# Kernel optimization log

Measured on AMD Instinct MI355X. Metric: run time of the kernel, lower is better.

Reference implementation:

```python
import jax, jax.numpy as jnp
import numpy as np

N, E, D_IN, D_H, D_OUT = 50000, 800000, 128, 128, 40
EPS = 1e-5


def setup_inputs() -> dict:
    key = jax.random.key(0)
    ks = jax.random.split(key, 12)
    x = jax.random.normal(ks[0], (N, D_IN), dtype=jnp.float32)
    edge_index = jax.random.randint(ks[1], (2, E), 0, N, dtype=jnp.int32)
    s = 1.0 / np.sqrt(D_H)
    return {
        "x": x,
        "edge_index": edge_index,
        "W1": jax.random.normal(ks[2], (D_IN, D_H), jnp.float32) * s,
        "b1": jnp.zeros((D_H,), jnp.float32),
        "W2": jax.random.normal(ks[3], (D_H, D_H), jnp.float32) * s,
        "b2": jnp.zeros((D_H,), jnp.float32),
        "g1": jnp.ones((D_H,), jnp.float32),
        "be1": jnp.zeros((D_H,), jnp.float32),
        "g2": jnp.ones((D_H,), jnp.float32),
        "be2": jnp.zeros((D_H,), jnp.float32),
        "g3": jnp.ones((D_H,), jnp.float32),
        "be3": jnp.zeros((D_H,), jnp.float32),
        "Wm": jax.random.normal(ks[4], (D_H, D_OUT), jnp.float32) * s,
        "bm": jnp.zeros((D_OUT,), jnp.float32),
    }


def _gcn_conv(x, W, b, src, dst, dinv):
    # GCNConv: x' = D^{-1/2}(A+I)D^{-1/2} (x W) + b
    xw = x @ W                                   # [N, H]
    coef = dinv[src] * dinv[dst]                 # [E]
    agg = jax.ops.segment_sum(xw[src] * coef[:, None], dst, num_segments=x.shape[0])
    agg = agg + xw * (dinv * dinv)[:, None]      # self-loop term
    return agg + b


def _bn(x, g, b):
    # BatchNorm1d in training mode: biased batch statistics over nodes
    m = jnp.mean(x, axis=0)
    v = jnp.var(x, axis=0)
    return g * (x - m) * jax.lax.rsqrt(v + EPS) + b


def reference(x, edge_index, W1, b1, W2, b2, g1, be1, g2, be2, g3, be3, Wm, bm):
    src, dst = edge_index[0], edge_index[1]
    # degree with self-loops (GCN symmetric normalization, computed on dst/col)
    deg = 1.0 + jax.ops.segment_sum(jnp.ones((E,), jnp.float32), dst, num_segments=N)
    dinv = jax.lax.rsqrt(deg)
    h = _gcn_conv(x, W1, b1, src, dst, dinv)
    h = jax.nn.relu(_bn(h, g1, be1))            # dropout is identity in eval
    h = _gcn_conv(h, W2, b2, src, dst, dinv)
    h = jax.nn.relu(_bn(h, g2, be2))
    h = _bn(h, g3, be3)
    h = h @ Wm + bm
    return jax.nn.log_softmax(h, axis=1)
```

## Files before the change

### kernel.cpp

```cpp
#include <hip/hip_runtime.h>
#include <hip/hip_fp16.h>
#include <math.h>

#define BN_EPS 1e-5f
#define CAP 128

typedef __attribute__((ext_vector_type(8))) short short8;
typedef __attribute__((ext_vector_type(4))) float floatx4;

__device__ inline unsigned short f2bf(float f) {
    union { float f; unsigned u; } x; x.f = f;
    unsigned r = x.u + 0x7fff + ((x.u >> 16) & 1);
    return (unsigned short)(r >> 16);
}
__device__ inline float bf2f(unsigned short h) {
    union { float f; unsigned u; } x; x.u = ((unsigned)h) << 16; return x.f;
}

__device__ inline void bn_sc_sh(float sum, float sumsq, float g, float be, float invN,
                                float& sc, float& sh) {
    float mean = sum * invN;
    float var = sumsq * invN - mean * mean;
    sc = g * rsqrtf(var + BN_EPS);
    sh = be - mean * sc;
}

__device__ inline void pack_one(int idx, const float* W1, const float* W2, const float* Wm,
                                unsigned short* p1, unsigned short* p2, unsigned short* pm) {
    const float* W;
    unsigned short* pack;
    int f, l = idx & 63, t, n, stride, ncols;
    if (idx < 2048) {
        W = W1; pack = p1; f = idx >> 6; t = f >> 3; n = (f & 7) * 16 + (l & 15);
        stride = 128; ncols = 128;
    } else if (idx < 4096) {
        W = W2; pack = p2; f = (idx - 2048) >> 6; t = f >> 3; n = (f & 7) * 16 + (l & 15);
        stride = 128; ncols = 128;
    } else {
        W = Wm; pack = pm; f = (idx - 4096) >> 6; t = f / 3; n = (f % 3) * 16 + (l & 15);
        stride = 40; ncols = 40;
    }
    int q = l >> 4;
    unsigned short* pp = pack + f * 1024 + l * 16;
#pragma unroll
    for (int j = 0; j < 8; ++j) {
        int k = t * 32 + q * 8 + j;
        float v = (n < ncols) ? W[k * stride + n] : 0.f;
        unsigned short hi = f2bf(v);
        float lo = v - bf2f(hi);
        pp[j] = hi;
        pp[8 + j] = f2bf(lo);
    }
}

__global__ void k_pack_fill(const float* __restrict__ W1, const float* __restrict__ W2,
                            const float* __restrict__ Wm, unsigned short* __restrict__ p1,
                            unsigned short* __restrict__ p2, unsigned short* __restrict__ pm,
                            const int* __restrict__ src, const int* __restrict__ dst, int E,
                            int* __restrict__ fillc, unsigned short* __restrict__ col16) {
    if (blockIdx.x < 19) {
        int idx = blockIdx.x * 256 + threadIdx.x;
        if (idx < 4864) pack_one(idx, W1, W2, Wm, p1, p2, pm);
        return;
    }
    int b = blockIdx.x - 19;
    int g = b & 7;
    int rank = b >> 3;
    int stride = ((gridDim.x - 19) >> 3) * 256;
    for (int e = rank * 256 + threadIdx.x; e < E; e += stride) {
        int d = dst[e];
        if ((d & 7) != g) continue;
        int r = atomicAdd(&fillc[d], 1);
        if (r < CAP) col16[(size_t)d * CAP + r] = (unsigned short)src[e];
    }
}

__device__ inline void load_row8(const float* arow, int kbase, float av[8]) {
    float4 a0 = *(const float4*)(arow + kbase);
    float4 a1 = *(const float4*)(arow + kbase + 4);
    av[0] = a0.x; av[1] = a0.y; av[2] = a0.z; av[3] = a0.w;
    av[4] = a1.x; av[5] = a1.y; av[6] = a1.z; av[7] = a1.w;
}
__device__ inline void load_row8(const __half* arow, int kbase, float av[8]) {
    float4 raw = *(const float4*)(arow + kbase);
    const __half2* h = (const __half2*)&raw;
#pragma unroll
    for (int i = 0; i < 4; ++i) {
        float2 f = __half22float2(h[i]);
        av[2 * i] = f.x;
        av[2 * i + 1] = f.y;
    }
}

template <typename T, bool FUSE_BN>
__global__ __launch_bounds__(256) void k_gemm_mfma(const T* __restrict__ A,
                                                   const unsigned short* __restrict__ packW,
                                                   const float* __restrict__ sums,
                                                   const float* __restrict__ g,
                                                   const float* __restrict__ be, float invN,
                                                   const int* __restrict__ fillc,
                                                   __half* __restrict__ C16, int M) {
    int lane = threadIdx.x & 63;
    int wv = threadIdx.x >> 6;
    int m0 = (blockIdx.x * 4 + wv) * 16;
    if (m0 >= M) return;
    int row = lane & 15, quad = lane >> 4;

    floatx4 acc[8];
#pragma unroll
    for (int nt = 0; nt < 8; ++nt) acc[nt] = (floatx4){0.f, 0.f, 0.f, 0.f};

    const T* arow = A + (size_t)(m0 + row) * 128;
#pragma unroll
    for (int t = 0; t < 4; ++t) {
        int kbase = t * 32 + quad * 8;
        float av[8];
        load_row8(arow, kbase, av);
        if (FUSE_BN) {
#pragma unroll
            for (int j = 0; j < 8; ++j) {
                int c = kbase + j;
                float sc, sh;
                bn_sc_sh(sums[c], sums[128 + c], g[c], be[c], invN, sc, sh);
                av[j] = fmaxf(av[j] * sc + sh, 0.f);
            }
        }
        short8 ah, al;
#pragma unroll
        for (int j = 0; j < 8; ++j) {
            unsigned short hi = f2bf(av[j]);
            ah[j] = (short)hi;
            al[j] = (short)f2bf(av[j] - bf2f(hi));
        }
        const unsigned short* wp = packW + (size_t)(t * 8) * 1024 + lane * 16;
#pragma unroll
        for (int nt = 0; nt < 8; ++nt) {
            short8 wh = *(const short8*)wp;
            short8 wl = *(const short8*)(wp + 8);
            wp += 1024;
            acc[nt] = __builtin_amdgcn_mfma_f32_16x16x32_bf16(ah, wh, acc[nt], 0, 0, 0);
            acc[nt] = __builtin_amdgcn_mfma_f32_16x16x32_bf16(al, wh, acc[nt], 0, 0, 0);
            acc[nt] = __builtin_amdgcn_mfma_f32_16x16x32_bf16(ah, wl, acc[nt], 0, 0, 0);
        }
    }

    float d[4];
#pragma unroll
    for (int r = 0; r < 4; ++r) d[r] = rsqrtf(1.f + (float)fillc[m0 + quad * 4 + r]);
#pragma unroll
    for (int nt = 0; nt < 8; ++nt) {
#pragma unroll
        for (int r = 0; r < 4; ++r) {
            C16[(size_t)(m0 + quad * 4 + r) * 128 + nt * 16 + row] =
                __float2half_rn(acc[nt][r] * d[r]);
        }
    }
}

__global__ __launch_bounds__(256) void k_gather(const __half2* __restrict__ y16,
                                                const int* __restrict__ fillc,
                                                const unsigned short* __restrict__ col16,
                                                const float* __restrict__ bias,
                                                __half2* __restrict__ out, int N) {
    int wv = threadIdx.x >> 6;
    int lane = threadIdx.x & 63;
    int n = blockIdx.x * 4 + wv;
    if (n >= N) return;
    float2 acc = __half22float2(y16[(size_t)n * 64 + lane]);
    int degraw = fillc[n];
    int deg = min(degraw, CAP);
    const unsigned short* cb = col16 + (size_t)n * CAP;
    for (int jb = 0; jb < deg; jb += 64) {
        int cnt = min(64, deg - jb);
        int idx = (lane < cnt) ? (int)cb[jb + lane] : 0;
        int jj = 0;
        for (; jj + 8 <= cnt; jj += 8) {
            int s0 = __shfl(idx, jj + 0, 64);
            int s1 = __shfl(idx, jj + 1, 64);
            int s2 = __shfl(idx, jj + 2, 64);
            int s3 = __shfl(idx, jj + 3, 64);
            int s4 = __shfl(idx, jj + 4, 64);
            int s5 = __shfl(idx, jj + 5, 64);
            int s6 = __shfl(idx, jj + 6, 64);
            int s7 = __shfl(idx, jj + 7, 64);
            float2 r0 = __half22float2(y16[(size_t)s0 * 64 + lane]);
            float2 r1 = __half22float2(y16[(size_t)s1 * 64 + lane]);
            float2 r2 = __half22float2(y16[(size_t)s2 * 64 + lane]);
            float2 r3 = __half22float2(y16[(size_t)s3 * 64 + lane]);
            float2 r4 = __half22float2(y16[(size_t)s4 * 64 + lane]);
            float2 r5 = __half22float2(y16[(size_t)s5 * 64 + lane]);
            float2 r6 = __half22float2(y16[(size_t)s6 * 64 + lane]);
            float2 r7 = __half22float2(y16[(size_t)s7 * 64 + lane]);
            acc.x += ((r0.x + r1.x) + (r2.x + r3.x)) + ((r4.x + r5.x) + (r6.x + r7.x));
            acc.y += ((r0.y + r1.y) + (r2.y + r3.y)) + ((r4.y + r5.y) + (r6.y + r7.y));
        }
        for (; jj < cnt; ++jj) {
            int s = __shfl(idx, jj, 64);
            float2 r = __half22float2(y16[(size_t)s * 64 + lane]);
            acc.x += r.x;
            acc.y += r.y;
        }
    }
    float dn = rsqrtf(1.f + (float)degraw);
    float2 b = *(const float2*)&bias[lane << 1];
    float2 o;
    o.x = dn * acc.x + b.x;
    o.y = dn * acc.y + b.y;
    out[(size_t)n * 64 + lane] = __float22half2_rn(o);
}

template <bool TRANSFORM>
__global__ __launch_bounds__(256) void k_stats(const __half2* __restrict__ h, int N,
                                               const float* __restrict__ sums2,
                                               const float* __restrict__ g2,
                                               const float* __restrict__ be2, float invN,
                                               float* __restrict__ stats) {
    int cp = threadIdx.x & 63;
    int rg = threadIdx.x >> 6;
    int rbeg = blockIdx.x * 256;
    int rend = min(rbeg + 256, N);
    float scx = 1.f, shx = 0.f, scy = 1.f, shy = 0.f;
    if (TRANSFORM) {
        int c = cp * 2;
        bn_sc_sh(sums2[c], sums2[128 + c], g2[c], be2[c], invN, scx, shx);
        bn_sc_sh(sums2[c + 1], sums2[128 + c + 1], g2[c + 1], be2[c + 1], invN, scy, shy);
    }
    float sx = 0.f, sy = 0.f, s2x = 0.f, s2y = 0.f;
    for (int r = rbeg + rg; r < rend; r += 4) {
        float2 v = __half22float2(h[(size_t)r * 64 + cp]);
        if (TRANSFORM) {
            v.x = fmaxf(v.x * scx + shx, 0.f);
            v.y = fmaxf(v.y * scy + shy, 0.f);
        }
        sx += v.x; sy += v.y;
        s2x += v.x * v.x; s2y += v.y * v.y;
    }
    __shared__ float ls[4][256];
    ls[0][threadIdx.x] = sx;
    ls[1][threadIdx.x] = sy;
    ls[2][threadIdx.x] = s2x;
    ls[3][threadIdx.x] = s2y;
    __syncthreads();
    if (threadIdx.x < 64) {
        int t = threadIdx.x;
        float a0 = ls[0][t] + ls[0][t + 64] + ls[0][t + 128] + ls[0][t + 192];
        float a1 = ls[1][t] + ls[1][t + 64] + ls[1][t + 128] + ls[1][t + 192];
        float a2 = ls[2][t] + ls[2][t + 64] + ls[2][t + 128] + ls[2][t + 192];
        float a3 = ls[3][t] + ls[3][t + 64] + ls[3][t + 128] + ls[3][t + 192];
        atomicAdd(&stats[2 * t], a0);
        atomicAdd(&stats[2 * t + 1], a1);
        atomicAdd(&stats[128 + 2 * t], a2);
        atomicAdd(&stats[128 + 2 * t + 1], a3);
    }
}

__global__ __launch_bounds__(256) void k_final(const __half* __restrict__ h,
                                               const float* __restrict__ sums2,
                                               const float* __restrict__ g2,
                                               const float* __restrict__ be2,
                                               const float* __restrict__ sums3,
                                               const float* __restrict__ g3,
                                               const float* __restrict__ be3, float invN,
                                               const unsigned short* __restrict__ packWm,
                                               const float* __restrict__ bm,
                                               float* __restrict__ out, int N) {
    int lane = threadIdx.x & 63;
    int wv = threadIdx.x >> 6;
    int m0 = (blockIdx.x * 4 + wv) * 16;
    if (m0 >= N) return;
    int row = lane & 15, quad = lane >> 4;

    floatx4 acc[3];
#pragma unroll
    for (int nt = 0; nt < 3; ++nt) acc[nt] = (floatx4){0.f, 0.f, 0.f, 0.f};

    const __half* arow = h + (size_t)(m0 + row) * 128;
#pragma unroll
    for (int t = 0; t < 4; ++t) {
        int kbase = t * 32 + quad * 8;
        float av[8];
        load_row8(arow, kbase, av);
#pragma unroll
        for (int j = 0; j < 8; ++j) {
            int c = kbase + j;
            float sc2, sh2, sc3, sh3;
            bn_sc_sh(sums2[c], sums2[128 + c], g2[c], be2[c], invN, sc2, sh2);
            bn_sc_sh(sums3[c], sums3[128 + c], g3[c], be3[c], invN, sc3, sh3);
            av[j] = fmaxf(av[j] * sc2 + sh2, 0.f) * sc3 + sh3;
        }
        short8 ah, al;
#pragma unroll
        for (int j = 0; j < 8; ++j) {
            unsigned short hi = f2bf(av[j]);
            ah[j] = (short)hi;
            al[j] = (short)f2bf(av[j] - bf2f(hi));
        }
        const unsigned short* wp = packWm + (size_t)(t * 3) * 1024 + lane * 16;
#pragma unroll
        for (int nt = 0; nt < 3; ++nt) {
            short8 wh = *(const short8*)wp;
            short8 wl = *(const short8*)(wp + 8);
            wp += 1024;
            acc[nt] = __builtin_amdgcn_mfma_f32_16x16x32_bf16(ah, wh, acc[nt], 0, 0, 0);
            acc[nt] = __builtin_amdgcn_mfma_f32_16x16x32_bf16(al, wh, acc[nt], 0, 0, 0);
            acc[nt] = __builtin_amdgcn_mfma_f32_16x16x32_bf16(ah, wl, acc[nt], 0, 0, 0);
        }
    }

    float bb[3];
#pragma unroll
    for (int nt = 0; nt < 3; ++nt) {
        int col = nt * 16 + row;
        bb[nt] = (col < 40) ? bm[col] : 0.f;
    }
    bool val2 = (row < 8);

#pragma unroll
    for (int r = 0; r < 4; ++r) {
        int m = m0 + quad * 4 + r;
        float v0 = acc[0][r] + bb[0];
        float v1 = acc[1][r] + bb[1];
        float v2 = acc[2][r] + bb[2];
        float mx = fmaxf(v0, v1);
        if (val2) mx = fmaxf(mx, v2);
#pragma unroll
        for (int off = 1; off <= 8; off <<= 1) mx = fmaxf(mx, __shfl_xor(mx, off, 64));
        float s = expf(v0 - mx) + expf(v1 - mx) + (val2 ? expf(v2 - mx) : 0.f);
#pragma unroll
        for (int off = 1; off <= 8; off <<= 1) s += __shfl_xor(s, off, 64);
        float lse = mx + logf(s);
        if (m < N) {
            out[(size_t)m * 40 + row] = v0 - lse;
            out[(size_t)m * 40 + 16 + row] = v1 - lse;
            if (val2) out[(size_t)m * 40 + 32 + row] = v2 - lse;
        }
    }
}

extern "C" void kernel_launch(void* const* d_in, const int* in_sizes, int n_in,
                              void* d_out, int out_size, void* d_ws, size_t ws_size,
                              hipStream_t stream) {
    const float* x   = (const float*)d_in[0];
    const int*   ei  = (const int*)d_in[1];
    const float* W1  = (const float*)d_in[2];
    const float* b1  = (const float*)d_in[3];
    const float* W2  = (const float*)d_in[4];
    const float* b2  = (const float*)d_in[5];
    const float* g1  = (const float*)d_in[6];
    const float* be1 = (const float*)d_in[7];
    const float* g2  = (const float*)d_in[8];
    const float* be2 = (const float*)d_in[9];
    const float* g3  = (const float*)d_in[10];
    const float* be3 = (const float*)d_in[11];
    const float* Wm  = (const float*)d_in[12];
    const float* bm  = (const float*)d_in[13];
    float* out = (float*)d_out;

    int N = in_sizes[0] / 128;
    int E = in_sizes[1] / 2;
    const int* srcs = ei;
    const int* dsts = ei + E;
    float invN = 1.0f / (float)N;

    char* ws = (char*)d_ws;
    size_t off = 0;
    auto alloc = [&](size_t bytes) -> void* {
        void* p = ws + off;
        off += (bytes + 255) & ~(size_t)255;
        return p;
    };
    size_t fill_rounded = (((size_t)N * 4) + 255) & ~(size_t)255;
    int*   fillc   = (int*)alloc((size_t)N * 4);
    float* statsAll= (float*)alloc(3 * 256 * 4);
    float* stats1  = statsAll;
    float* stats2  = statsAll + 256;
    float* stats3  = statsAll + 512;
    unsigned short* col16 = (unsigned short*)alloc((size_t)N * CAP * 2);
    unsigned short* packW1 = (unsigned short*)alloc(32768 * 2);
    unsigned short* packW2 = (unsigned short*)alloc(32768 * 2);
    unsigned short* packWm = (unsigned short*)alloc(12288 * 2);
    __half* y16 = (__half*)alloc((size_t)N * 128 * 2);
    __half* h16 = (__half*)alloc((size_t)N * 128 * 2);
    (void)ws_size; (void)n_in; (void)out_size;

    hipMemsetAsync(fillc, 0, fill_rounded + 3 * 256 * 4, stream);

    int nthb = (N + 255) / 256;
    int gb = (N + 63) / 64;
    int gatherb = (N + 3) / 4;

    k_pack_fill<<<19 + 1024, 256, 0, stream>>>(W1, W2, Wm, packW1, packW2, packWm, srcs, dsts,
                                               E, fillc, col16);

    k_gemm_mfma<float, false><<<gb, 256, 0, stream>>>(x, packW1, nullptr, nullptr, nullptr,
                                                      invN, fillc, y16, N);
    k_gather<<<gatherb, 256, 0, stream>>>((const __half2*)y16, fillc, col16, b1,
                                          (__half2*)h16, N);
    k_stats<false><<<nthb, 256, 0, stream>>>((const __half2*)h16, N, nullptr, nullptr, nullptr,
                                             invN, stats1);

    k_gemm_mfma<__half, true><<<gb, 256, 0, stream>>>(h16, packW2, stats1, g1, be1, invN,
                                                      fillc, y16, N);
    k_gather<<<gatherb, 256, 0, stream>>>((const __half2*)y16, fillc, col16, b2,
                                          (__half2*)h16, N);
    k_stats<false><<<nthb, 256, 0, stream>>>((const __half2*)h16, N, nullptr, nullptr, nullptr,
                                             invN, stats2);

    k_stats<true><<<nthb, 256, 0, stream>>>((const __half2*)h16, N, stats2, g2, be2, invN,
                                            stats3);
    k_final<<<gb, 256, 0, stream>>>(h16, stats2, g2, be2, stats3, g3, be3, invN, packWm, bm,
                                    out, N);
}
```

Before: 318.1 us.

## Overlap CSR fill with first GEMM by moving dinv scaling into gather

```diff
diff --git a/kernel.cpp b/kernel.cpp
--- a/kernel.cpp
+++ b/kernel.cpp
@@ -53,20 +53,130 @@
     }
 }
 
-__global__ void k_pack_fill(const float* __restrict__ W1, const float* __restrict__ W2,
-                            const float* __restrict__ Wm, unsigned short* __restrict__ p1,
-                            unsigned short* __restrict__ p2, unsigned short* __restrict__ pm,
-                            const int* __restrict__ src, const int* __restrict__ dst, int E,
-                            int* __restrict__ fillc, unsigned short* __restrict__ col16) {
+__global__ __launch_bounds__(256) void k_pre(const float* __restrict__ W1,
+                                             const float* __restrict__ W2,
+                                             const float* __restrict__ Wm,
+                                             unsigned short* __restrict__ p1,
+                                             unsigned short* __restrict__ p2,
+                                             unsigned short* __restrict__ pm,
+                                             int4* __restrict__ zdst, int nz4) {
     if (blockIdx.x < 19) {
         int idx = blockIdx.x * 256 + threadIdx.x;
         if (idx < 4864) pack_one(idx, W1, W2, Wm, p1, p2, pm);
         return;
     }
-    int b = blockIdx.x - 19;
+    int i = (blockIdx.x - 19) * 256 + threadIdx.x;
+    if (i < nz4) zdst[i] = make_int4(0, 0, 0, 0);
+}
+
+__device__ inline void load_row8(const float* arow, int kbase, float av[8]) {
+    float4 a0 = *(const float4*)(arow + kbase);
+    float4 a1 = *(const float4*)(arow + kbase + 4);
+    av[0] = a0.x; av[1] = a0.y; av[2] = a0.z; av[3] = a0.w;
+    av[4] = a1.x; av[5] = a1.y; av[6] = a1.z; av[7] = a1.w;
+}
+__device__ inline void load_row8(const __half* arow, int kbase, float av[8]) {
+    float4 raw = *(const float4*)(arow + kbase);
+    const __half2* h = (const __half2*)&raw;
+#pragma unroll
+    for (int i = 0; i < 4; ++i) {
+        float2 f = __half22float2(h[i]);
+        av[2 * i] = f.x;
+        av[2 * i + 1] = f.y;
+    }
+}
+
+template <typename T, bool FUSE_BN>
+__device__ __forceinline__ void gemm_body(int bid, const T* __restrict__ A,
+                                          const unsigned short* __restrict__ packW,
+                                          const float* __restrict__ sums,
+                                          const float* __restrict__ g,
+                                          const float* __restrict__ be, float invN,
+                                          __half* __restrict__ C16, int M) {
+    int lane = threadIdx.x & 63;
+    int wv = threadIdx.x >> 6;
+    int m0 = (bid * 4 + wv) * 32;
+    if (m0 >= M) return;
+    int row = lane & 15, quad = lane >> 4;
+    bool has2 = (m0 + 16 < M);
+
+    floatx4 acc0[8], acc1[8];
+#pragma unroll
+    for (int nt = 0; nt < 8; ++nt) {
+        acc0[nt] = (floatx4){0.f, 0.f, 0.f, 0.f};
+        acc1[nt] = (floatx4){0.f, 0.f, 0.f, 0.f};
+    }
+
+    const T* arow0 = A + (size_t)(m0 + row) * 128;
+    const T* arow1 = A + (size_t)((has2 ? m0 + 16 : m0) + row) * 128;
+#pragma unroll
+    for (int t = 0; t < 4; ++t) {
+        int kbase = t * 32 + quad * 8;
+        float av0[8], av1[8];
+        load_row8(arow0, kbase, av0);
+        load_row8(arow1, kbase, av1);
+        if (FUSE_BN) {
+#pragma unroll
+            for (int j = 0; j < 8; ++j) {
+                int c = kbase + j;
+                float sc, sh;
+                bn_sc_sh(sums[c], sums[128 + c], g[c], be[c], invN, sc, sh);
+                av0[j] = fmaxf(av0[j] * sc + sh, 0.f);
+                av1[j] = fmaxf(av1[j] * sc + sh, 0.f);
+            }
+        }
+        short8 ah0, al0, ah1, al1;
+#pragma unroll
+        for (int j = 0; j < 8; ++j) {
+            unsigned short hi0 = f2bf(av0[j]);
+            ah0[j] = (short)hi0;
+            al0[j] = (short)f2bf(av0[j] - bf2f(hi0));
+            unsigned short hi1 = f2bf(av1[j]);
+            ah1[j] = (short)hi1;
+            al1[j] = (short)f2bf(av1[j] - bf2f(hi1));
+        }
+        const unsigned short* wp = packW + (size_t)(t * 8) * 1024 + lane * 16;
+#pragma unroll
+        for (int nt = 0; nt < 8; ++nt) {
+            short8 wh = *(const short8*)wp;
+            short8 wl = *(const short8*)(wp + 8);
+            wp += 1024;
+            acc0[nt] = __builtin_amdgcn_mfma_f32_16x16x32_bf16(ah0, wh, acc0[nt], 0, 0, 0);
+            acc0[nt] = __builtin_amdgcn_mfma_f32_16x16x32_bf16(al0, wh, acc0[nt], 0, 0, 0);
+            acc0[nt] = __builtin_amdgcn_mfma_f32_16x16x32_bf16(ah0, wl, acc0[nt], 0, 0, 0);
+            acc1[nt] = __builtin_amdgcn_mfma_f32_16x16x32_bf16(ah1, wh, acc1[nt], 0, 0, 0);
+            acc1[nt] = __builtin_amdgcn_mfma_f32_16x16x32_bf16(al1, wh, acc1[nt], 0, 0, 0);
+            acc1[nt] = __builtin_amdgcn_mfma_f32_16x16x32_bf16(ah1, wl, acc1[nt], 0, 0, 0);
+        }
+    }
+
+#pragma unroll
+    for (int nt = 0; nt < 8; ++nt) {
+#pragma unroll
+        for (int r = 0; r < 4; ++r) {
+            C16[(size_t)(m0 + quad * 4 + r) * 128 + nt * 16 + row] =
+                __float2half_rn(acc0[nt][r]);
+        }
+    }
+    if (has2) {
+#pragma unroll
+        for (int nt = 0; nt < 8; ++nt) {
+#pragma unroll
+            for (int r = 0; r < 4; ++r) {
+                C16[(size_t)(m0 + 16 + quad * 4 + r) * 128 + nt * 16 + row] =
+                    __float2half_rn(acc1[nt][r]);
+            }
+        }
+    }
+}
+
+__device__ __forceinline__ void fill_body(int b, const int* __restrict__ src,
+                                          const int* __restrict__ dst, int E,
+                                          int* __restrict__ fillc,
+                                          unsigned short* __restrict__ col16, int nfill) {
     int g = b & 7;
     int rank = b >> 3;
-    int stride = ((gridDim.x - 19) >> 3) * 256;
+    int stride = (nfill >> 3) * 256;
     for (int e = rank * 256 + threadIdx.x; e < E; e += stride) {
         int d = dst[e];
         if ((d & 7) != g) continue;
@@ -75,86 +185,29 @@
     }
 }
 
-__device__ inline void load_row8(const float* arow, int kbase, float av[8]) {
-    float4 a0 = *(const float4*)(arow + kbase);
-    float4 a1 = *(const float4*)(arow + kbase + 4);
-    av[0] = a0.x; av[1] = a0.y; av[2] = a0.z; av[3] = a0.w;
-    av[4] = a1.x; av[5] = a1.y; av[6] = a1.z; av[7] = a1.w;
-}
-__device__ inline void load_row8(const __half* arow, int kbase, float av[8]) {
-    float4 raw = *(const float4*)(arow + kbase);
-    const __half2* h = (const __half2*)&raw;
-#pragma unroll
-    for (int i = 0; i < 4; ++i) {
-        float2 f = __half22float2(h[i]);
-        av[2 * i] = f.x;
-        av[2 * i + 1] = f.y;
-    }
+__global__ __launch_bounds__(256) void k_fill_gemm1(const float* __restrict__ x,
+                                                    const unsigned short* __restrict__ packW1,
+                                                    __half* __restrict__ y16, int M, int ngemm,
+                                                    const int* __restrict__ src,
+                                                    const int* __restrict__ dst, int E,
+                                                    int* __restrict__ fillc,
+                                                    unsigned short* __restrict__ col16,
+                                                    int nfill) {
+    if ((int)blockIdx.x < ngemm) {
+        gemm_body<float, false>(blockIdx.x, x, packW1, nullptr, nullptr, nullptr, 0.f, y16, M);
+        return;
+    }
+    fill_body((int)blockIdx.x - ngemm, src, dst, E, fillc, col16, nfill);
 }
 
 template <typename T, bool FUSE_BN>
-__global__ __launch_bounds__(256) void k_gemm_mfma(const T* __restrict__ A,
-                                                   const unsigned short* __restrict__ packW,
-                                                   const float* __restrict__ sums,
-                                                   const float* __restrict__ g,
-                                                   const float* __restrict__ be, float invN,
-                                                   const int* __restrict__ fillc,
-                                                   __half* __restrict__ C16, int M) {
-    int lane = threadIdx.x & 63;
-    int wv = threadIdx.x >> 6;
-    int m0 = (blockIdx.x * 4 + wv) * 16;
-    if (m0 >= M) return;
-    int row = lane & 15, quad = lane >> 4;
-
-    floatx4 acc[8];
-#pragma unroll
-    for (int nt = 0; nt < 8; ++nt) acc[nt] = (floatx4){0.f, 0.f, 0.f, 0.f};
-
-    const T* arow = A + (size_t)(m0 + row) * 128;
-#pragma unroll
-    for (int t = 0; t < 4; ++t) {
-        int kbase = t * 32 + quad * 8;
-        float av[8];
-        load_row8(arow, kbase, av);
-        if (FUSE_BN) {
-#pragma unroll
-            for (int j = 0; j < 8; ++j) {
-                int c = kbase + j;
-                float sc, sh;
-                bn_sc_sh(sums[c], sums[128 + c], g[c], be[c], invN, sc, sh);
-                av[j] = fmaxf(av[j] * sc + sh, 0.f);
-            }
-        }
-        short8 ah, al;
-#pragma unroll
-        for (int j = 0; j < 8; ++j) {
-            unsigned short hi = f2bf(av[j]);
-            ah[j] = (short)hi;
-            al[j] = (short)f2bf(av[j] - bf2f(hi));
-        }
-        const unsigned short* wp = packW + (size_t)(t * 8) * 1024 + lane * 16;
-#pragma unroll
-        for (int nt = 0; nt < 8; ++nt) {
-            short8 wh = *(const short8*)wp;
-            short8 wl = *(const short8*)(wp + 8);
-            wp += 1024;
-            acc[nt] = __builtin_amdgcn_mfma_f32_16x16x32_bf16(ah, wh, acc[nt], 0, 0, 0);
-            acc[nt] = __builtin_amdgcn_mfma_f32_16x16x32_bf16(al, wh, acc[nt], 0, 0, 0);
-            acc[nt] = __builtin_amdgcn_mfma_f32_16x16x32_bf16(ah, wl, acc[nt], 0, 0, 0);
-        }
-    }
-
-    float d[4];
-#pragma unroll
-    for (int r = 0; r < 4; ++r) d[r] = rsqrtf(1.f + (float)fillc[m0 + quad * 4 + r]);
-#pragma unroll
-    for (int nt = 0; nt < 8; ++nt) {
-#pragma unroll
-        for (int r = 0; r < 4; ++r) {
-            C16[(size_t)(m0 + quad * 4 + r) * 128 + nt * 16 + row] =
-                __float2half_rn(acc[nt][r] * d[r]);
-        }
-    }
+__global__ __launch_bounds__(256) void k_gemm(const T* __restrict__ A,
+                                              const unsigned short* __restrict__ packW,
+                                              const float* __restrict__ sums,
+                                              const float* __restrict__ g,
+                                              const float* __restrict__ be, float invN,
+                                              __half* __restrict__ C16, int M) {
+    gemm_body<T, FUSE_BN>(blockIdx.x, A, packW, sums, g, be, invN, C16, M);
 }
 
 __global__ __launch_bounds__(256) void k_gather(const __half2* __restrict__ y16,
@@ -166,13 +219,18 @@
     int lane = threadIdx.x & 63;
     int n = blockIdx.x * 4 + wv;
     if (n >= N) return;
-    float2 acc = __half22float2(y16[(size_t)n * 64 + lane]);
     int degraw = fillc[n];
+    float dn = rsqrtf(1.f + (float)degraw);
+    float2 self = __half22float2(y16[(size_t)n * 64 + lane]);
+    float2 acc;
+    acc.x = dn * self.x;
+    acc.y = dn * self.y;
     int deg = min(degraw, CAP);
     const unsigned short* cb = col16 + (size_t)n * CAP;
     for (int jb = 0; jb < deg; jb += 64) {
         int cnt = min(64, deg - jb);
         int idx = (lane < cnt) ? (int)cb[jb + lane] : 0;
+        float dv = (lane < cnt) ? rsqrtf(1.f + (float)fillc[idx]) : 0.f;
         int jj = 0;
         for (; jj + 8 <= cnt; jj += 8) {
             int s0 = __shfl(idx, jj + 0, 64);
@@ -183,6 +241,14 @@
             int s5 = __shfl(idx, jj + 5, 64);
             int s6 = __shfl(idx, jj + 6, 64);
             int s7 = __shfl(idx, jj + 7, 64);
+            float w0 = __shfl(dv, jj + 0, 64);
+            float w1 = __shfl(dv, jj + 1, 64);
+            float w2 = __shfl(dv, jj + 2, 64);
+            float w3 = __shfl(dv, jj + 3, 64);
+            float w4 = __shfl(dv, jj + 4, 64);
+            float w5 = __shfl(dv, jj + 5, 64);
+            float w6 = __shfl(dv, jj + 6, 64);
+            float w7 = __shfl(dv, jj + 7, 64);
             float2 r0 = __half22float2(y16[(size_t)s0 * 64 + lane]);
             float2 r1 = __half22float2(y16[(size_t)s1 * 64 + lane]);
             float2 r2 = __half22float2(y16[(size_t)s2 * 64 + lane]);
@@ -191,17 +257,19 @@
             float2 r5 = __half22float2(y16[(size_t)s5 * 64 + lane]);
             float2 r6 = __half22float2(y16[(size_t)s6 * 64 + lane]);
             float2 r7 = __half22float2(y16[(size_t)s7 * 64 + lane]);
-            acc.x += ((r0.x + r1.x) + (r2.x + r3.x)) + ((r4.x + r5.x) + (r6.x + r7.x));
-            acc.y += ((r0.y + r1.y) + (r2.y + r3.y)) + ((r4.y + r5.y) + (r6.y + r7.y));
+            acc.x += w0 * r0.x + w1 * r1.x + w2 * r2.x + w3 * r3.x +
+                     w4 * r4.x + w5 * r5.x + w6 * r6.x + w7 * r7.x;
+            acc.y += w0 * r0.y + w1 * r1.y + w2 * r2.y + w3 * r3.y +
+                     w4 * r4.y + w5 * r5.y + w6 * r6.y + w7 * r7.y;
         }
         for (; jj < cnt; ++jj) {
             int s = __shfl(idx, jj, 64);
+            float w = __shfl(dv, jj, 64);
             float2 r = __half22float2(y16[(size_t)s * 64 + lane]);
-            acc.x += r.x;
-            acc.y += r.y;
-        }
-    }
-    float dn = rsqrtf(1.f + (float)degraw);
+            acc.x += w * r.x;
+            acc.y += w * r.y;
+        }
+    }
     float2 b = *(const float2*)&bias[lane << 1];
     float2 o;
     o.x = dn * acc.x + b.x;
@@ -383,24 +451,28 @@
     __half* h16 = (__half*)alloc((size_t)N * 128 * 2);
     (void)ws_size; (void)n_in; (void)out_size;
 
-    hipMemsetAsync(fillc, 0, fill_rounded + 3 * 256 * 4, stream);
-
     int nthb = (N + 255) / 256;
-    int gb = (N + 63) / 64;
     int gatherb = (N + 3) / 4;
-
-    k_pack_fill<<<19 + 1024, 256, 0, stream>>>(W1, W2, Wm, packW1, packW2, packWm, srcs, dsts,
-                                               E, fillc, col16);
-
-    k_gemm_mfma<float, false><<<gb, 256, 0, stream>>>(x, packW1, nullptr, nullptr, nullptr,
-                                                      invN, fillc, y16, N);
+    int gfb = (N + 63) / 64;
+    int ngemm = (N + 127) / 128;
+    const int NFILL = 1024;
+
+    int nz4 = (int)((fill_rounded + 3 * 256 * 4) / 16);
+    int zb = (nz4 + 255) / 256;
+
+    k_pre<<<19 + zb, 256, 0, stream>>>(W1, W2, Wm, packW1, packW2, packWm,
+                                       (int4*)fillc, nz4);
+
+    k_fill_gemm1<<<ngemm + NFILL, 256, 0, stream>>>(x, packW1, y16, N, ngemm, srcs, dsts, E,
+                                                    fillc, col16, NFILL);
+
     k_gather<<<gatherb, 256, 0, stream>>>((const __half2*)y16, fillc, col16, b1,
                                           (__half2*)h16, N);
     k_stats<false><<<nthb, 256, 0, stream>>>((const __half2*)h16, N, nullptr, nullptr, nullptr,
                                              invN, stats1);
 
-    k_gemm_mfma<__half, true><<<gb, 256, 0, stream>>>(h16, packW2, stats1, g1, be1, invN,
-                                                      fillc, y16, N);
+    k_gemm<__half, true><<<ngemm, 256, 0, stream>>>(h16, packW2, stats1, g1, be1, invN,
+                                                    y16, N);
     k_gather<<<gatherb, 256, 0, stream>>>((const __half2*)y16, fillc, col16, b2,
                                           (__half2*)h16, N);
     k_stats<false><<<nthb, 256, 0, stream>>>((const __half2*)h16, N, nullptr, nullptr, nullptr,
@@ -408,6 +480,6 @@
 
     k_stats<true><<<nthb, 256, 0, stream>>>((const __half2*)h16, N, stats2, g2, be2, invN,
                                             stats3);
-    k_final<<<gb, 256, 0, stream>>>(h16, stats2, g2, be2, stats3, g3, be3, invN, packWm, bm,
-                                    out, N);
-}
+    k_final<<<gfb, 256, 0, stream>>>(h16, stats2, g2, be2, stats3, g3, be3, invN, packWm, bm,
+                                     out, N);
+}
```

New measurement: 320.5 us. About the same (+0.8%).

## Split pack/fill kernel, zero buffers in-kernel, raise fill grid, preload GEMM rows

Applied to the files above, without the earlier changes.

```diff
diff --git a/kernel.cpp b/kernel.cpp
--- a/kernel.cpp
+++ b/kernel.cpp
@@ -53,20 +53,30 @@
     }
 }
 
-__global__ void k_pack_fill(const float* __restrict__ W1, const float* __restrict__ W2,
-                            const float* __restrict__ Wm, unsigned short* __restrict__ p1,
-                            unsigned short* __restrict__ p2, unsigned short* __restrict__ pm,
-                            const int* __restrict__ src, const int* __restrict__ dst, int E,
-                            int* __restrict__ fillc, unsigned short* __restrict__ col16) {
+__global__ __launch_bounds__(256) void k_pre(const float* __restrict__ W1,
+                                             const float* __restrict__ W2,
+                                             const float* __restrict__ Wm,
+                                             unsigned short* __restrict__ p1,
+                                             unsigned short* __restrict__ p2,
+                                             unsigned short* __restrict__ pm,
+                                             int4* __restrict__ zdst, int nz4) {
     if (blockIdx.x < 19) {
         int idx = blockIdx.x * 256 + threadIdx.x;
         if (idx < 4864) pack_one(idx, W1, W2, Wm, p1, p2, pm);
         return;
     }
-    int b = blockIdx.x - 19;
+    int i = (blockIdx.x - 19) * 256 + threadIdx.x;
+    if (i < nz4) zdst[i] = make_int4(0, 0, 0, 0);
+}
+
+__global__ __launch_bounds__(256) void k_fill(const int* __restrict__ src,
+                                              const int* __restrict__ dst, int E,
+                                              int* __restrict__ fillc,
+                                              unsigned short* __restrict__ col16, int nfill) {
+    int b = (int)blockIdx.x;
     int g = b & 7;
     int rank = b >> 3;
-    int stride = ((gridDim.x - 19) >> 3) * 256;
+    int stride = (nfill >> 3) * 256;
     for (int e = rank * 256 + threadIdx.x; e < E; e += stride) {
         int d = dst[e];
         if ((d & 7) != g) continue;
@@ -93,16 +103,16 @@
 }
 
 template <typename T, bool FUSE_BN>
-__global__ __launch_bounds__(256) void k_gemm_mfma(const T* __restrict__ A,
-                                                   const unsigned short* __restrict__ packW,
-                                                   const float* __restrict__ sums,
-                                                   const float* __restrict__ g,
-                                                   const float* __restrict__ be, float invN,
-                                                   const int* __restrict__ fillc,
-                                                   __half* __restrict__ C16, int M) {
+__global__ __launch_bounds__(256) void k_gemm(const T* __restrict__ A,
+                                              const unsigned short* __restrict__ packW,
+                                              const float* __restrict__ sums,
+                                              const float* __restrict__ g,
+                                              const float* __restrict__ be, float invN,
+                                              const int* __restrict__ fillc,
+                                              __half* __restrict__ C16, int M) {
     int lane = threadIdx.x & 63;
     int wv = threadIdx.x >> 6;
-    int m0 = (blockIdx.x * 4 + wv) * 16;
+    int m0 = ((int)blockIdx.x * 4 + wv) * 16;
     if (m0 >= M) return;
     int row = lane & 15, quad = lane >> 4;
 
@@ -111,26 +121,29 @@
     for (int nt = 0; nt < 8; ++nt) acc[nt] = (floatx4){0.f, 0.f, 0.f, 0.f};
 
     const T* arow = A + (size_t)(m0 + row) * 128;
+
+    float av[4][8];
+#pragma unroll
+    for (int t = 0; t < 4; ++t) load_row8(arow, t * 32 + quad * 8, av[t]);
+
 #pragma unroll
     for (int t = 0; t < 4; ++t) {
         int kbase = t * 32 + quad * 8;
-        float av[8];
-        load_row8(arow, kbase, av);
         if (FUSE_BN) {
 #pragma unroll
             for (int j = 0; j < 8; ++j) {
                 int c = kbase + j;
                 float sc, sh;
                 bn_sc_sh(sums[c], sums[128 + c], g[c], be[c], invN, sc, sh);
-                av[j] = fmaxf(av[j] * sc + sh, 0.f);
+                av[t][j] = fmaxf(av[t][j] * sc + sh, 0.f);
             }
         }
         short8 ah, al;
 #pragma unroll
         for (int j = 0; j < 8; ++j) {
-            unsigned short hi = f2bf(av[j]);
+            unsigned short hi = f2bf(av[t][j]);
             ah[j] = (short)hi;
-            al[j] = (short)f2bf(av[j] - bf2f(hi));
+            al[j] = (short)f2bf(av[t][j] - bf2f(hi));
         }
         const unsigned short* wp = packW + (size_t)(t * 8) * 1024 + lane * 16;
 #pragma unroll
@@ -266,7 +279,7 @@
                                                float* __restrict__ out, int N) {
     int lane = threadIdx.x & 63;
     int wv = threadIdx.x >> 6;
-    int m0 = (blockIdx.x * 4 + wv) * 16;
+    int m0 = ((int)blockIdx.x * 4 + wv) * 16;
     if (m0 >= N) return;
     int row = lane & 15, quad = lane >> 4;
 
@@ -275,25 +288,28 @@
     for (int nt = 0; nt < 3; ++nt) acc[nt] = (floatx4){0.f, 0.f, 0.f, 0.f};
 
     const __half* arow = h + (size_t)(m0 + row) * 128;
+
+    float av[4][8];
+#pragma unroll
+    for (int t = 0; t < 4; ++t) load_row8(arow, t * 32 + quad * 8, av[t]);
+
 #pragma unroll
     for (int t = 0; t < 4; ++t) {
         int kbase = t * 32 + quad * 8;
-        float av[8];
-        load_row8(arow, kbase, av);
 #pragma unroll
         for (int j = 0; j < 8; ++j) {
             int c = kbase + j;
             float sc2, sh2, sc3, sh3;
             bn_sc_sh(sums2[c], sums2[128 + c], g2[c], be2[c], invN, sc2, sh2);
             bn_sc_sh(sums3[c], sums3[128 + c], g3[c], be3[c], invN, sc3, sh3);
-            av[j] = fmaxf(av[j] * sc2 + sh2, 0.f) * sc3 + sh3;
+            av[t][j] = fmaxf(av[t][j] * sc2 + sh2, 0.f) * sc3 + sh3;
         }
         short8 ah, al;
 #pragma unroll
         for (int j = 0; j < 8; ++j) {
-            unsigned short hi = f2bf(av[j]);
+            unsigned short hi = f2bf(av[t][j]);
             ah[j] = (short)hi;
-            al[j] = (short)f2bf(av[j] - bf2f(hi));
+            al[j] = (short)f2bf(av[t][j] - bf2f(hi));
         }
         const unsigned short* wp = packWm + (size_t)(t * 3) * 1024 + lane * 16;
 #pragma unroll
@@ -383,24 +399,29 @@
     __half* h16 = (__half*)alloc((size_t)N * 128 * 2);
     (void)ws_size; (void)n_in; (void)out_size;
 
-    hipMemsetAsync(fillc, 0, fill_rounded + 3 * 256 * 4, stream);
-
     int nthb = (N + 255) / 256;
-    int gb = (N + 63) / 64;
     int gatherb = (N + 3) / 4;
-
-    k_pack_fill<<<19 + 1024, 256, 0, stream>>>(W1, W2, Wm, packW1, packW2, packWm, srcs, dsts,
-                                               E, fillc, col16);
-
-    k_gemm_mfma<float, false><<<gb, 256, 0, stream>>>(x, packW1, nullptr, nullptr, nullptr,
-                                                      invN, fillc, y16, N);
+    int ngemm = (N + 63) / 64;
+    int gfb = (N + 63) / 64;
+    const int NFILL = 8192;
+
+    int nz4 = (int)((fill_rounded + 3 * 256 * 4) / 16);
+    int zb = (nz4 + 255) / 256;
+
+    k_pre<<<19 + zb, 256, 0, stream>>>(W1, W2, Wm, packW1, packW2, packWm,
+                                       (int4*)fillc, nz4);
+
+    k_fill<<<NFILL, 256, 0, stream>>>(srcs, dsts, E, fillc, col16, NFILL);
+
+    k_gemm<float, false><<<ngemm, 256, 0, stream>>>(x, packW1, nullptr, nullptr, nullptr,
+                                                    invN, fillc, y16, N);
     k_gather<<<gatherb, 256, 0, stream>>>((const __half2*)y16, fillc, col16, b1,
                                           (__half2*)h16, N);
     k_stats<false><<<nthb, 256, 0, stream>>>((const __half2*)h16, N, nullptr, nullptr, nullptr,
                                              invN, stats1);
 
-    k_gemm_mfma<__half, true><<<gb, 256, 0, stream>>>(h16, packW2, stats1, g1, be1, invN,
-                                                      fillc, y16, N);
+    k_gemm<__half, true><<<ngemm, 256, 0, stream>>>(h16, packW2, stats1, g1, be1, invN,
+                                                    fillc, y16, N);
     k_gather<<<gatherb, 256, 0, stream>>>((const __half2*)y16, fillc, col16, b2,
                                           (__half2*)h16, N);
     k_stats<false><<<nthb, 256, 0, stream>>>((const __half2*)h16, N, nullptr, nullptr, nullptr,
@@ -408,6 +429,6 @@
 
     k_stats<true><<<nthb, 256, 0, stream>>>((const __half2*)h16, N, stats2, g2, be2, invN,
                                             stats3);
-    k_final<<<gb, 256, 0, stream>>>(h16, stats2, g2, be2, stats3, g3, be3, invN, packWm, bm,
-                                    out, N);
-}
+    k_final<<<gfb, 256, 0, stream>>>(h16, stats2, g2, be2, stats3, g3, be3, invN, packWm, bm,
+                                     out, N);
+}
```

After: 322.0 us. Within noise of the previous version (+1.2%).
